# Performance work log

Hardware: AMD Instinct MI355X
Metric: run time of the kernel (lower is better)

## Reference

```python
import jax, jax.numpy as jnp
import numpy as np

N = 10000      # nodes
E = 320000     # edges (avg degree 32)
D_IN = 128
D_H = 256
D_C = 32       # comm_dim
D_OUT = 64


def setup_inputs() -> dict:
    key = jax.random.key(0)
    ks = jax.random.split(key, 14)
    p = lambda k, shape: jax.random.normal(k, shape, jnp.float32) * 0.02
    return {
        "x": jax.random.normal(ks[0], (N, D_IN), jnp.float32),
        "edge_index": jax.random.randint(ks[1], (2, E), 0, N),
        "W_in": p(ks[2], (D_IN, D_H)), "b_in": jnp.zeros((D_H,), jnp.float32),
        "Wq": p(ks[3], (D_H, D_C)),   "bq": jnp.zeros((D_C,), jnp.float32),
        "Wk": p(ks[4], (D_H, D_C)),   "bk": jnp.zeros((D_C,), jnp.float32),
        "Wv": p(ks[5], (D_H, D_H)),   "bv": jnp.zeros((D_H,), jnp.float32),
        "W1": p(ks[6], (2 * D_H, D_H)), "b1": jnp.zeros((D_H,), jnp.float32),
        "W2": p(ks[7], (D_H, D_OUT)),  "b2": jnp.zeros((D_OUT,), jnp.float32),
    }


def reference(x, edge_index, W_in, b_in, Wq, bq, Wk, bk, Wv, bv, W1, b1, W2, b2):
    n = x.shape[0]
    h = x @ W_in + b_in                       # [N, D_H]
    q = h @ Wq + bq                           # [N, D_C]
    k = h @ Wk + bk                           # [N, D_C]
    v = h @ Wv + bv                           # [N, D_H]
    scores = (q @ k.T) / np.sqrt(q.shape[-1]).astype(np.float32)  # [N, N]
    # torch: zeros -> scatter 1 at edges -> masked_fill(==0, -inf);
    # edge positions keep value 1.0 ADDED to scores (faithful quirk).
    mask = jnp.full((n, n), -jnp.inf, jnp.float32)
    mask = mask.at[edge_index[0], edge_index[1]].set(1.0)
    w = jax.nn.softmax(scores + mask, axis=-1)
    w = jnp.nan_to_num(w, nan=0.0)            # rows with no edges -> all zeros
    comm = w @ v                              # [N, D_H]
    combined = jnp.concatenate([h, comm], axis=-1)  # [N, 2*D_H]
    return jax.nn.relu(combined @ W1 + b1) @ W2 + b2  # [N, D_OUT]
```

## Files before the change

### kernel.cpp

```cpp
#include <hip/hip_runtime.h>
#include <stdint.h>
#include <stddef.h>

constexpr int N_NODES = 10000;
constexpr int N_EDGES = 320000;
constexpr int DIM_IN  = 128;
constexpr int DIM_H   = 256;
constexpr int DIM_C   = 32;
constexpr int DIM_OUT = 64;
constexpr int DIM_QKV = DIM_C + DIM_C + DIM_H;
constexpr int DIM_QK  = 2 * DIM_C;
constexpr int DIM_CAT = 2 * DIM_H;
constexpr float SCALE = 0.17677669529663687f;
constexpr int MAXD = 192;
constexpr float VSCALE = 64.0f;
constexpr int PAD2 = 72;
constexpr int HP   = 264;

#if __has_builtin(__builtin_amdgcn_cvt_pk_f32_fp8) && __has_builtin(__builtin_amdgcn_cvt_pk_f32_fp8)
#define V_FP8 1
#else
#define V_FP8 0
#endif

constexpr size_t alignw(size_t w) { return (w + 15) & ~size_t(15); }
constexpr size_t OFF_DEG   = 0;
constexpr size_t OFF_COL   = alignw(OFF_DEG + N_NODES);
constexpr size_t OFF_QK    = alignw(OFF_COL + (size_t)N_NODES * MAXD);
constexpr size_t OFF_VT    = alignw(OFF_QK + (size_t)N_NODES * DIM_QK);
constexpr size_t OFF_CATBF = alignw(OFF_VT + (size_t)N_NODES * DIM_H / 2);
constexpr size_t OFF_WINT  = alignw(OFF_CATBF + (size_t)N_NODES * DIM_CAT / 2);
constexpr size_t OFF_WQKVT = alignw(OFF_WINT + (size_t)DIM_H * DIM_IN / 2);
constexpr size_t OFF_W1T   = alignw(OFF_WQKVT + (size_t)DIM_QKV * DIM_H / 2);
constexpr size_t OFF_W2T   = alignw(OFF_W1T + (size_t)DIM_H * DIM_CAT / 2);

typedef __attribute__((ext_vector_type(8))) short short8;
typedef __attribute__((ext_vector_type(4))) float floatx4;
typedef __attribute__((ext_vector_type(2))) float floatx2;

#define MFMA16 __builtin_amdgcn_mfma_f32_16x16x32_bf16

__device__ inline unsigned short f2bf(float f) {
    uint32_t u = __builtin_bit_cast(uint32_t, f);
    uint32_t r = (u + 0x7fffu + ((u >> 16) & 1u)) >> 16;
    return (unsigned short)r;
}
__device__ inline float bf2f_lo(uint32_t u) { return __builtin_bit_cast(float, u << 16); }
__device__ inline float bf2f_hi(uint32_t u) { return __builtin_bit_cast(float, u & 0xffff0000u); }

__global__ void prep_w(const float* __restrict__ W_in,
                       const float* __restrict__ Wq, const float* __restrict__ Wk,
                       const float* __restrict__ Wv,
                       int* __restrict__ deg,
                       unsigned short* __restrict__ WinT, unsigned short* __restrict__ WqkvT)
{
    const int i0 = blockIdx.x * blockDim.x + threadIdx.x;
    const int stride = gridDim.x * blockDim.x;
    for (int i = i0; i < N_NODES; i += stride) deg[i] = 0;
    for (int idx = i0; idx < DIM_IN * DIM_H; idx += stride) {
        int k = idx >> 8, n = idx & 255;
        WinT[n * DIM_IN + k] = f2bf(W_in[idx]);
    }
    for (int idx = i0; idx < DIM_H * DIM_C; idx += stride) {
        int k = idx >> 5, n = idx & 31;
        WqkvT[n * DIM_H + k] = f2bf(Wq[idx]);
    }
    for (int idx = i0; idx < DIM_H * DIM_C; idx += stride) {
        int k = idx >> 5, n = idx & 31;
        WqkvT[(DIM_C + n) * DIM_H + k] = f2bf(Wk[idx]);
    }
    for (int idx = i0; idx < DIM_H * DIM_H; idx += stride) {
        int k = idx >> 8, n = idx & 255;
        WqkvT[(2 * DIM_C + n) * DIM_H + k] = f2bf(Wv[idx]);
    }
}

__global__ __launch_bounds__(256)
void gemm12(const float* __restrict__ x, const int* __restrict__ ei,
            const unsigned short* __restrict__ WinT, const float* __restrict__ b_in,
            const unsigned short* __restrict__ WqkvT,
            const float* __restrict__ bq, const float* __restrict__ bk,
            const float* __restrict__ bv,
            const float* __restrict__ W1, const float* __restrict__ W2,
            int* __restrict__ deg, int* __restrict__ col,
            unsigned short* __restrict__ cat_bf, float* __restrict__ qk,
            unsigned short* __restrict__ v_tab,
            unsigned short* __restrict__ W1T, unsigned short* __restrict__ W2T)
{
    __shared__ alignas(16) char SMEM[62976];
    short* hS  = (short*)SMEM;
    short* As1 = (short*)(SMEM + 16896);
    short* Bs1 = (short*)(SMEM + 21504);
    short* Bs2 = (short*)(SMEM + 16896);
    const int tid   = threadIdx.x;
    const int bid   = blockIdx.x;
    const int wave  = tid >> 6;
    const int lane  = tid & 63;
    const int quad  = lane >> 4;
    const int col16 = lane & 15;
    const int sr    = tid >> 3;
    const int sc    = (tid & 7) * 8;
    const int row0  = bid * 32;
    const int gr_s  = row0 + sr;

    float4 xa = {}, xb = {};
    if (gr_s < N_NODES) {
        const float4* xp = (const float4*)(x + (size_t)gr_s * DIM_IN + sc);
        xa = xp[0]; xb = xp[1];
    }
    short8 wreg[8];
    #pragma unroll
    for (int p = 0; p < 8; ++p)
        wreg[p] = *(const short8*)(WinT + (size_t)(sr + p * 32) * DIM_IN + sc);

    short8 breg[10];
    floatx4 acc[2][4] = {};
    #pragma unroll
    for (int k0 = 0; k0 < DIM_IN; k0 += 64) {
        {
            uint4 o;
            o.x = (uint32_t)f2bf(xa.x) | ((uint32_t)f2bf(xa.y) << 16);
            o.y = (uint32_t)f2bf(xa.z) | ((uint32_t)f2bf(xa.w) << 16);
            o.z = (uint32_t)f2bf(xb.x) | ((uint32_t)f2bf(xb.y) << 16);
            o.w = (uint32_t)f2bf(xb.z) | ((uint32_t)f2bf(xb.w) << 16);
            *(uint4*)(As1 + sr * PAD2 + sc) = o;
        }
        #pragma unroll
        for (int p = 0; p < 8; ++p)
            *(short8*)(Bs1 + (sr + p * 32) * PAD2 + sc) = wreg[p];
        if (k0 + 64 < DIM_IN) {
            xa = {}; xb = {};
            if (gr_s < N_NODES) {
                const float4* xp = (const float4*)(x + (size_t)gr_s * DIM_IN + (k0 + 64) + sc);
                xa = xp[0]; xb = xp[1];
            }
            #pragma unroll
            for (int p = 0; p < 8; ++p)
                wreg[p] = *(const short8*)(WinT + (size_t)(sr + p * 32) * DIM_IN + (k0 + 64) + sc);
        } else {
            #pragma unroll
            for (int p = 0; p < 10; ++p)
                breg[p] = *(const short8*)(WqkvT + (size_t)(sr + p * 32) * DIM_H + sc);
        }
        __syncthreads();
        short8 af[2][2], bfr[4][2];
        #pragma unroll
        for (int m = 0; m < 2; ++m)
            #pragma unroll
            for (int kh = 0; kh < 2; ++kh)
                af[m][kh] = *(const short8*)(As1 + (m * 16 + col16) * PAD2 + kh * 32 + quad * 8);
        #pragma unroll
        for (int n = 0; n < 4; ++n)
            #pragma unroll
            for (int kh = 0; kh < 2; ++kh)
                bfr[n][kh] = *(const short8*)(Bs1 + (wave * 64 + n * 16 + col16) * PAD2 + kh * 32 + quad * 8);
        #pragma unroll
        for (int m = 0; m < 2; ++m)
            #pragma unroll
            for (int n = 0; n < 4; ++n)
                #pragma unroll
                for (int kh = 0; kh < 2; ++kh)
                    acc[m][n] = MFMA16(af[m][kh], bfr[n][kh], acc[m][n], 0, 0, 0);
        __syncthreads();
    }
    #pragma unroll
    for (int m = 0; m < 2; ++m)
        #pragma unroll
        for (int n = 0; n < 4; ++n) {
            int gc = wave * 64 + n * 16 + col16;
            float bia = b_in[gc];
            #pragma unroll
            for (int r = 0; r < 4; ++r) {
                int lr = m * 16 + quad * 4 + r;
                unsigned short hv = f2bf(acc[m][n][r] + bia);
                hS[lr * HP + gc] = (short)hv;
                if (row0 + lr < N_NODES) cat_bf[(size_t)(row0 + lr) * DIM_CAT + gc] = hv;
            }
        }
    __syncthreads();

    floatx4 acc2[2][5] = {};
    #pragma unroll
    for (int k0 = 0; k0 < DIM_H; k0 += 64) {
        #pragma unroll
        for (int p = 0; p < 10; ++p)
            *(short8*)(Bs2 + (sr + p * 32) * PAD2 + sc) = breg[p];
        if (k0 + 64 < DIM_H) {
            #pragma unroll
            for (int p = 0; p < 10; ++p)
                breg[p] = *(const short8*)(WqkvT + (size_t)(sr + p * 32) * DIM_H + (k0 + 64) + sc);
        }
        __syncthreads();
        short8 af[2][2], bfr[5][2];
        #pragma unroll
        for (int m = 0; m < 2; ++m)
            #pragma unroll
            for (int kh = 0; kh < 2; ++kh)
                af[m][kh] = *(const short8*)(hS + (m * 16 + col16) * HP + k0 + kh * 32 + quad * 8);
        #pragma unroll
        for (int n = 0; n < 5; ++n)
            #pragma unroll
            for (int kh = 0; kh < 2; ++kh)
                bfr[n][kh] = *(const short8*)(Bs2 + (wave * 80 + n * 16 + col16) * PAD2 + kh * 32 + quad * 8);
        #pragma unroll
        for (int m = 0; m < 2; ++m)
            #pragma unroll
            for (int n = 0; n < 5; ++n)
                #pragma unroll
                for (int kh = 0; kh < 2; ++kh)
                    acc2[m][n] = MFMA16(af[m][kh], bfr[n][kh], acc2[m][n], 0, 0, 0);
        __syncthreads();
    }
    #pragma unroll
    for (int m = 0; m < 2; ++m)
        #pragma unroll
        for (int n = 0; n < 5; ++n) {
            int gc = wave * 80 + n * 16 + col16;
            float bia = (gc < DIM_C) ? bq[gc] : (gc < DIM_QK) ? bk[gc - DIM_C] : bv[gc - DIM_QK];
            #pragma unroll
            for (int r = 0; r < 4; ++r) {
                int gr = row0 + m * 16 + quad * 4 + r;
                if (gr >= N_NODES) continue;
                float v = acc2[m][n][r] + bia;
                if (gc < DIM_QK) {
                    qk[(size_t)gr * DIM_QK + gc] = v;
                } else {
#if V_FP8
                    int pk = __builtin_amdgcn_cvt_pk_fp8_f32(v * VSCALE, 0.f, 0, false);
                    ((unsigned char*)v_tab)[(size_t)gr * DIM_H + (gc - DIM_QK)] =
                        (unsigned char)(pk & 0xff);
#else
                    v_tab[(size_t)gr * DIM_H + (gc - DIM_QK)] = f2bf(v);
#endif
                }
            }
        }

    {
        const int stride = gridDim.x * 256;
        const int i0 = bid * 256 + tid;
        int s4[4], d4[4]; bool ok[4];
        #pragma unroll
        for (int t = 0; t < 4; ++t) {
            int e = i0 + t * stride;
            ok[t] = e < N_EDGES;
            s4[t] = ok[t] ? ei[e] : 0;
            d4[t] = ok[t] ? ei[N_EDGES + e] : 0;
        }
        #pragma unroll
        for (int t = 0; t < 4; ++t)
            if (ok[t]) {
                int slot = atomicAdd(&deg[s4[t]], 1);
                if (slot < MAXD) col[s4[t] * MAXD + slot] = d4[t];
            }
        for (int idx = i0; idx < DIM_CAT * DIM_H; idx += stride) {
            int k = idx >> 8, n = idx & 255;
            W1T[n * DIM_CAT + k] = f2bf(W1[idx]);
        }
        for (int idx = i0; idx < DIM_H * DIM_OUT; idx += stride) {
            int k = idx >> 6, n = idx & 63;
            W2T[n * DIM_H + k] = f2bf(W2[idx]);
        }
    }
}

__global__ __launch_bounds__(256)
void attn_row(const float* __restrict__ qk, const unsigned short* __restrict__ v_tab,
              const int* __restrict__ deg, const int* __restrict__ col,
              unsigned short* __restrict__ cat_bf) {
    __shared__ alignas(16) int dstS[4][MAXD];
    __shared__ float wS[4][MAXD];
    __shared__ float qS[4][DIM_C];
    const int wave = threadIdx.x >> 6;
    const int lane = threadIdx.x & 63;
    const int row = blockIdx.x * 4 + wave;
    int d = deg[row];
    if (d > MAXD) d = MAXD;
    const int* crow = col + (size_t)row * MAXD;

    for (int p = lane; p < d; p += 64) dstS[wave][p] = crow[p];
    if (lane < DIM_C) qS[wave][lane] = qk[(size_t)row * DIM_QK + lane];
    __syncthreads();

    float mysum = 0.f;
    if (d <= 64) {
        int mydst = (lane < d) ? dstS[wave][lane] : -1;
        bool dup = false;
        {
            const int4* ds4 = (const int4*)(&dstS[wave][0]);
            const int lim = (lane < d) ? lane : 0;
            for (int j0 = 0; j0 < lim; j0 += 4) {
                int4 v = ds4[j0 >> 2];
                dup = dup || (v.x == mydst)
                   || (j0 + 1 < lim && v.y == mydst)
                   || (j0 + 2 < lim && v.z == mydst)
                   || (j0 + 3 < lim && v.w == mydst);
            }
        }
        float w = 0.f;
        if (lane < d && !dup) {
            const float4* kp = (const float4*)(qk + (size_t)mydst * DIM_QK + DIM_C);
            float s = 0.f;
            #pragma unroll
            for (int i = 0; i < DIM_C / 4; ++i) {
                float4 b = kp[i];
                s += qS[wave][4 * i + 0] * b.x + qS[wave][4 * i + 1] * b.y
                   + qS[wave][4 * i + 2] * b.z + qS[wave][4 * i + 3] * b.w;
            }
            w = expf(s * SCALE);
        }
        wS[wave][lane] = w;
        mysum = w;
    } else {
        for (int p = lane; p < d; p += 64) {
            int mydst = dstS[wave][p];
            bool dup = false;
            for (int j = 0; j < p; ++j) dup = dup || (dstS[wave][j] == mydst);
            float w = 0.f;
            if (!dup) {
                const float4* kp = (const float4*)(qk + (size_t)mydst * DIM_QK + DIM_C);
                float s = 0.f;
                #pragma unroll
                for (int i = 0; i < DIM_C / 4; ++i) {
                    float4 b = kp[i];
                    s += qS[wave][4 * i + 0] * b.x + qS[wave][4 * i + 1] * b.y
                       + qS[wave][4 * i + 2] * b.z + qS[wave][4 * i + 3] * b.w;
                }
                w = expf(s * SCALE);
            }
            wS[wave][p] = w;
            mysum += w;
        }
    }
    #pragma unroll
    for (int off = 32; off; off >>= 1) mysum += __shfl_down(mysum, off, 64);
    float total = __shfl(mysum, 0, 64);
#if V_FP8
    float inv = (d > 0 && total > 0.f) ? 1.0f / (total * VSCALE) : 0.f;
#else
    float inv = (d > 0 && total > 0.f) ? 1.0f / total : 0.f;
#endif
    __syncthreads();

    float4 acc = make_float4(0.f, 0.f, 0.f, 0.f);
#if V_FP8
    const uint32_t* vb = (const uint32_t*)v_tab;
#else
    const uint2* vb = (const uint2*)v_tab;
#endif
    for (int p0 = 0; p0 < d; p0 += 16) {
        int j[16]; float w[16];
        #pragma unroll
        for (int t = 0; t < 16; ++t) {
            int idx = p0 + t;
            bool in = idx < d;
            j[t] = in ? dstS[wave][idx] : 0;
            w[t] = in ? wS[wave][idx] : 0.f;
        }
#if V_FP8
        uint32_t r[16];
        #pragma unroll
        for (int t = 0; t < 16; ++t) r[t] = vb[(size_t)j[t] * 64 + lane];
        #pragma unroll
        for (int t = 0; t < 16; ++t) {
            floatx2 lo = __builtin_amdgcn_cvt_pk_f32_fp8(r[t], false);
            floatx2 hi = __builtin_amdgcn_cvt_pk_f32_fp8(r[t], true);
            acc.x += w[t] * lo.x; acc.y += w[t] * lo.y;
            acc.z += w[t] * hi.x; acc.w += w[t] * hi.y;
        }
#else
        uint2 r[16];
        #pragma unroll
        for (int t = 0; t < 16; ++t) r[t] = vb[(size_t)j[t] * 64 + lane];
        #pragma unroll
        for (int t = 0; t < 16; ++t) {
            acc.x += w[t] * bf2f_lo(r[t].x);
            acc.y += w[t] * bf2f_hi(r[t].x);
            acc.z += w[t] * bf2f_lo(r[t].y);
            acc.w += w[t] * bf2f_hi(r[t].y);
        }
#endif
    }
    acc.x *= inv; acc.y *= inv; acc.z *= inv; acc.w *= inv;
    uint2 o;
    o.x = (uint32_t)f2bf(acc.x) | ((uint32_t)f2bf(acc.y) << 16);
    o.y = (uint32_t)f2bf(acc.z) | ((uint32_t)f2bf(acc.w) << 16);
    *(uint2*)(cat_bf + (size_t)row * DIM_CAT + DIM_H + lane * 4) = o;
}

__global__ __launch_bounds__(256)
void gemm_w1w2(const unsigned short* __restrict__ cat, const unsigned short* __restrict__ W1T,
               const float* __restrict__ b1, const unsigned short* __restrict__ W2T,
               const float* __restrict__ b2, float* __restrict__ out, int M)
{
    constexpr int TP = 260;
    __shared__ short As[32 * PAD2];
    __shared__ short BsTs[256 * PAD2];
    short* Bs = BsTs;
    short* Ts = BsTs;
    const int tid   = threadIdx.x;
    const int wave  = tid >> 6;
    const int lane  = tid & 63;
    const int quad  = lane >> 4;
    const int col16 = lane & 15;
    const int row0  = blockIdx.x * 32;

    const int sr = tid >> 3;
    const int sc = (tid & 7) * 8;
    const int gr_s = row0 + sr;

    short8 areg = {};
    if (gr_s < M) areg = *(const short8*)(cat + (size_t)gr_s * DIM_CAT + sc);
    short8 breg[8];
    #pragma unroll
    for (int p = 0; p < 8; ++p)
        breg[p] = *(const short8*)(W1T + (size_t)(sr + p * 32) * DIM_CAT + sc);

    floatx4 acc[2][4] = {};
    #pragma unroll
    for (int k0 = 0; k0 < DIM_CAT; k0 += 64) {
        *(short8*)(As + sr * PAD2 + sc) = areg;
        #pragma unroll
        for (int p = 0; p < 8; ++p)
            *(short8*)(Bs + (sr + p * 32) * PAD2 + sc) = breg[p];
        if (k0 + 64 < DIM_CAT) {
            areg = short8{};
            if (gr_s < M) areg = *(const short8*)(cat + (size_t)gr_s * DIM_CAT + (k0 + 64) + sc);
            #pragma unroll
            for (int p = 0; p < 8; ++p)
                breg[p] = *(const short8*)(W1T + (size_t)(sr + p * 32) * DIM_CAT + (k0 + 64) + sc);
        }
        __syncthreads();
        short8 af[2][2], bfr[4][2];
        #pragma unroll
        for (int m = 0; m < 2; ++m)
            #pragma unroll
            for (int kh = 0; kh < 2; ++kh)
                af[m][kh] = *(const short8*)(As + (m * 16 + col16) * PAD2 + kh * 32 + quad * 8);
        #pragma unroll
        for (int n = 0; n < 4; ++n)
            #pragma unroll
            for (int kh = 0; kh < 2; ++kh)
                bfr[n][kh] = *(const short8*)(Bs + (wave * 64 + n * 16 + col16) * PAD2 + kh * 32 + quad * 8);
        #pragma unroll
        for (int m = 0; m < 2; ++m)
            #pragma unroll
            for (int n = 0; n < 4; ++n)
                #pragma unroll
                for (int kh = 0; kh < 2; ++kh)
                    acc[m][n] = MFMA16(af[m][kh], bfr[n][kh], acc[m][n], 0, 0, 0);
        __syncthreads();
    }

    #pragma unroll
    for (int m = 0; m < 2; ++m)
        #pragma unroll
        for (int n = 0; n < 4; ++n) {
            int gc = wave * 64 + n * 16 + col16;
            float bia = b1[gc];
            #pragma unroll
            for (int r = 0; r < 4; ++r) {
                int lr = m * 16 + quad * 4 + r;
                Ts[lr * TP + gc] = (short)f2bf(fmaxf(acc[m][n][r] + bia, 0.f));
            }
        }
    __syncthreads();

    floatx4 acc2[2] = {};
    #pragma unroll
    for (int k0 = 0; k0 < DIM_H; k0 += 32) {
        short8 b = *(const short8*)(W2T + (size_t)(wave * 16 + col16) * DIM_H + k0 + quad * 8);
        #pragma unroll
        for (int m = 0; m < 2; ++m) {
            short8 a = *(const short8*)(Ts + (m * 16 + col16) * TP + k0 + quad * 8);
            acc2[m] = MFMA16(a, b, acc2[m], 0, 0, 0);
        }
    }
    #pragma unroll
    for (int m = 0; m < 2; ++m) {
        int gc = wave * 16 + col16;
        float bia = b2[gc];
        #pragma unroll
        for (int r = 0; r < 4; ++r) {
            int gr = row0 + m * 16 + quad * 4 + r;
            if (gr < M) out[(size_t)gr * DIM_OUT + gc] = acc2[m][r] + bia;
        }
    }
}

extern "C" void kernel_launch(void* const* d_in, const int* in_sizes, int n_in,
                              void* d_out, int out_size, void* d_ws, size_t ws_size,
                              hipStream_t stream) {
    (void)in_sizes; (void)n_in; (void)out_size; (void)ws_size;
    const float* x    = (const float*)d_in[0];
    const int*   ei   = (const int*)d_in[1];
    const float* W_in = (const float*)d_in[2];
    const float* b_in = (const float*)d_in[3];
    const float* Wq   = (const float*)d_in[4];
    const float* bq   = (const float*)d_in[5];
    const float* Wk   = (const float*)d_in[6];
    const float* bk   = (const float*)d_in[7];
    const float* Wv   = (const float*)d_in[8];
    const float* bv   = (const float*)d_in[9];
    const float* W1   = (const float*)d_in[10];
    const float* b1   = (const float*)d_in[11];
    const float* W2   = (const float*)d_in[12];
    const float* b2   = (const float*)d_in[13];
    float* out = (float*)d_out;

    uint32_t* ws      = (uint32_t*)d_ws;
    int*      deg     = (int*)(ws + OFF_DEG);
    int*      col     = (int*)(ws + OFF_COL);
    float*    qk      = (float*)(ws + OFF_QK);
    unsigned short* v_tab  = (unsigned short*)(ws + OFF_VT);
    unsigned short* cat_bf = (unsigned short*)(ws + OFF_CATBF);
    unsigned short* WinT   = (unsigned short*)(ws + OFF_WINT);
    unsigned short* WqkvT  = (unsigned short*)(ws + OFF_WQKVT);
    unsigned short* W1T    = (unsigned short*)(ws + OFF_W1T);
    unsigned short* W2T    = (unsigned short*)(ws + OFF_W2T);

    prep_w<<<256, 256, 0, stream>>>(W_in, Wq, Wk, Wv, deg, WinT, WqkvT);
    gemm12<<<(N_NODES + 31) / 32, 256, 0, stream>>>(
        x, ei, WinT, b_in, WqkvT, bq, bk, bv, W1, W2,
        deg, col, cat_bf, qk, v_tab, W1T, W2T);
    attn_row<<<N_NODES / 4, 256, 0, stream>>>(qk, v_tab, deg, col, cat_bf);
    gemm_w1w2<<<(N_NODES + 31) / 32, 256, 0, stream>>>(
        cat_bf, W1T, b1, W2T, b2, out, N_NODES);
}
```

Measured before the change: 162.1 us.

## Fold W_in into QKV and W1 weights to skip materializing h

Exploits linearity: h = x·W_in + b_in is never formed. A prep kernel precomputes W_in·[Wq|Wk|Wv] and W_in·W1[:256], plus the matching effective biases. The QKV GEMM then runs with K=128 directly on x, and the W1 GEMM uses K=384 over x and comm. This removes the h GEMM and the cat buffer writes, but adds a small fp32 weight-product prep and changes bf16 rounding, since the product is rounded once instead of h being rounded.

New measurement: 165.6 us. 1.02x slower.

```diff
diff --git a/kernel.cpp b/kernel.cpp
--- a/kernel.cpp
+++ b/kernel.cpp
@@ -10,14 +10,13 @@
 constexpr int DIM_OUT = 64;
 constexpr int DIM_QKV = DIM_C + DIM_C + DIM_H;
 constexpr int DIM_QK  = 2 * DIM_C;
-constexpr int DIM_CAT = 2 * DIM_H;
+constexpr int K_W1    = DIM_IN + DIM_H;
 constexpr float SCALE = 0.17677669529663687f;
 constexpr int MAXD = 192;
 constexpr float VSCALE = 64.0f;
 constexpr int PAD2 = 72;
-constexpr int HP   = 264;
-
-#if __has_builtin(__builtin_amdgcn_cvt_pk_f32_fp8) && __has_builtin(__builtin_amdgcn_cvt_pk_f32_fp8)
+
+#if __has_builtin(__builtin_amdgcn_cvt_pk_f32_fp8) && __has_builtin(__builtin_amdgcn_cvt_pk_fp8_f32)
 #define V_FP8 1
 #else
 #define V_FP8 0
@@ -28,11 +27,12 @@
 constexpr size_t OFF_COL   = alignw(OFF_DEG + N_NODES);
 constexpr size_t OFF_QK    = alignw(OFF_COL + (size_t)N_NODES * MAXD);
 constexpr size_t OFF_VT    = alignw(OFF_QK + (size_t)N_NODES * DIM_QK);
-constexpr size_t OFF_CATBF = alignw(OFF_VT + (size_t)N_NODES * DIM_H / 2);
-constexpr size_t OFF_WINT  = alignw(OFF_CATBF + (size_t)N_NODES * DIM_CAT / 2);
-constexpr size_t OFF_WQKVT = alignw(OFF_WINT + (size_t)DIM_H * DIM_IN / 2);
-constexpr size_t OFF_W1T   = alignw(OFF_WQKVT + (size_t)DIM_QKV * DIM_H / 2);
-constexpr size_t OFF_W2T   = alignw(OFF_W1T + (size_t)DIM_H * DIM_CAT / 2);
+constexpr size_t OFF_CMB   = alignw(OFF_VT + (size_t)N_NODES * DIM_H / 2);
+constexpr size_t OFF_WEFF  = alignw(OFF_CMB + (size_t)N_NODES * DIM_H / 2);
+constexpr size_t OFF_W1BIG = alignw(OFF_WEFF + (size_t)DIM_QKV * DIM_IN / 2);
+constexpr size_t OFF_W2T   = alignw(OFF_W1BIG + (size_t)DIM_H * K_W1 / 2);
+constexpr size_t OFF_BEFF  = alignw(OFF_W2T + (size_t)DIM_OUT * DIM_H / 2);
+constexpr size_t OFF_B1EFF = alignw(OFF_BEFF + DIM_QKV);
 
 typedef __attribute__((ext_vector_type(8))) short short8;
 typedef __attribute__((ext_vector_type(4))) float floatx4;
@@ -48,50 +48,87 @@
 __device__ inline float bf2f_lo(uint32_t u) { return __builtin_bit_cast(float, u << 16); }
 __device__ inline float bf2f_hi(uint32_t u) { return __builtin_bit_cast(float, u & 0xffff0000u); }
 
-__global__ void prep_w(const float* __restrict__ W_in,
-                       const float* __restrict__ Wq, const float* __restrict__ Wk,
-                       const float* __restrict__ Wv,
-                       int* __restrict__ deg,
-                       unsigned short* __restrict__ WinT, unsigned short* __restrict__ WqkvT)
+__global__ __launch_bounds__(320)
+void prep(const float* __restrict__ W_in,
+          const float* __restrict__ Wq, const float* __restrict__ Wk,
+          const float* __restrict__ Wv,
+          const float* __restrict__ bq, const float* __restrict__ bk,
+          const float* __restrict__ bv, const float* __restrict__ b_in,
+          const float* __restrict__ W1, const float* __restrict__ b1,
+          const float* __restrict__ W2,
+          int* __restrict__ deg,
+          unsigned short* __restrict__ WeffT, unsigned short* __restrict__ W1big,
+          unsigned short* __restrict__ W2T,
+          float* __restrict__ b_eff, float* __restrict__ b1_eff)
 {
-    const int i0 = blockIdx.x * blockDim.x + threadIdx.x;
-    const int stride = gridDim.x * blockDim.x;
-    for (int i = i0; i < N_NODES; i += stride) deg[i] = 0;
-    for (int idx = i0; idx < DIM_IN * DIM_H; idx += stride) {
-        int k = idx >> 8, n = idx & 255;
-        WinT[n * DIM_IN + k] = f2bf(W_in[idx]);
-    }
-    for (int idx = i0; idx < DIM_H * DIM_C; idx += stride) {
-        int k = idx >> 5, n = idx & 31;
-        WqkvT[n * DIM_H + k] = f2bf(Wq[idx]);
-    }
-    for (int idx = i0; idx < DIM_H * DIM_C; idx += stride) {
-        int k = idx >> 5, n = idx & 31;
-        WqkvT[(DIM_C + n) * DIM_H + k] = f2bf(Wk[idx]);
-    }
-    for (int idx = i0; idx < DIM_H * DIM_H; idx += stride) {
-        int k = idx >> 8, n = idx & 255;
-        WqkvT[(2 * DIM_C + n) * DIM_H + k] = f2bf(Wv[idx]);
+    const int bid = blockIdx.x;
+    const int tid = threadIdx.x;
+    if (bid < 128) {
+        const int k = bid, n = tid;
+        float acc = 0.f;
+        const float* wrow = W_in + (size_t)k * DIM_H;
+        if (n < DIM_C) {
+            for (int j = 0; j < DIM_H; ++j) acc += wrow[j] * Wq[j * DIM_C + n];
+        } else if (n < DIM_QK) {
+            for (int j = 0; j < DIM_H; ++j) acc += wrow[j] * Wk[j * DIM_C + (n - DIM_C)];
+        } else {
+            for (int j = 0; j < DIM_H; ++j) acc += wrow[j] * Wv[j * DIM_H + (n - DIM_QK)];
+        }
+        WeffT[n * DIM_IN + k] = f2bf(acc);
+    } else if (bid < 256) {
+        const int k = bid - 128, n = tid;
+        if (n < DIM_H) {
+            float acc = 0.f;
+            const float* wrow = W_in + (size_t)k * DIM_H;
+            for (int j = 0; j < DIM_H; ++j) acc += wrow[j] * W1[(size_t)j * DIM_H + n];
+            W1big[n * K_W1 + k] = f2bf(acc);
+        }
+    } else if (bid < 288) {
+        for (int idx = (bid - 256) * 320 + tid; idx < DIM_H * DIM_H; idx += 32 * 320) {
+            int jj = idx >> 8, n = idx & 255;
+            W1big[n * K_W1 + DIM_IN + jj] = f2bf(W1[(size_t)(DIM_H + jj) * DIM_H + n]);
+        }
+    } else if (bid < 296) {
+        for (int idx = (bid - 288) * 320 + tid; idx < DIM_H * DIM_OUT; idx += 8 * 320) {
+            int k = idx >> 6, n = idx & 63;
+            W2T[n * DIM_H + k] = f2bf(W2[(size_t)k * DIM_OUT + n]);
+        }
+    } else if (bid == 296) {
+        const int n = tid;
+        float acc;
+        if (n < DIM_C) {
+            acc = bq[n];
+            for (int j = 0; j < DIM_H; ++j) acc += b_in[j] * Wq[j * DIM_C + n];
+        } else if (n < DIM_QK) {
+            acc = bk[n - DIM_C];
+            for (int j = 0; j < DIM_H; ++j) acc += b_in[j] * Wk[j * DIM_C + (n - DIM_C)];
+        } else {
+            acc = bv[n - DIM_QK];
+            for (int j = 0; j < DIM_H; ++j) acc += b_in[j] * Wv[j * DIM_H + (n - DIM_QK)];
+        }
+        b_eff[n] = acc;
+    } else if (bid == 297) {
+        const int n = tid;
+        if (n < DIM_H) {
+            float acc = b1[n];
+            for (int j = 0; j < DIM_H; ++j) acc += b_in[j] * W1[(size_t)j * DIM_H + n];
+            b1_eff[n] = acc;
+        }
+    } else {
+        int i = (bid - 298) * 320 + tid;
+        if (i < N_NODES) deg[i] = 0;
     }
 }
 
 __global__ __launch_bounds__(256)
-void gemm12(const float* __restrict__ x, const int* __restrict__ ei,
-            const unsigned short* __restrict__ WinT, const float* __restrict__ b_in,
-            const unsigned short* __restrict__ WqkvT,
-            const float* __restrict__ bq, const float* __restrict__ bk,
-            const float* __restrict__ bv,
-            const float* __restrict__ W1, const float* __restrict__ W2,
-            int* __restrict__ deg, int* __restrict__ col,
-            unsigned short* __restrict__ cat_bf, float* __restrict__ qk,
-            unsigned short* __restrict__ v_tab,
-            unsigned short* __restrict__ W1T, unsigned short* __restrict__ W2T)
+void gemm_qkv(const float* __restrict__ x, const int* __restrict__ ei,
+              const unsigned short* __restrict__ WeffT, const float* __restrict__ b_eff,
+              int* __restrict__ deg, int* __restrict__ col,
+              float* __restrict__ qk, unsigned short* __restrict__ v_tab)
 {
-    __shared__ alignas(16) char SMEM[62976];
-    short* hS  = (short*)SMEM;
-    short* As1 = (short*)(SMEM + 16896);
-    short* Bs1 = (short*)(SMEM + 21504);
-    short* Bs2 = (short*)(SMEM + 16896);
+    __shared__ alignas(16) char SMEM[50688];
+    short* As = (short*)SMEM;
+    short* Bs = (short*)(SMEM + 4608);
     const int tid   = threadIdx.x;
     const int bid   = blockIdx.x;
     const int wave  = tid >> 6;
@@ -108,13 +145,12 @@
         const float4* xp = (const float4*)(x + (size_t)gr_s * DIM_IN + sc);
         xa = xp[0]; xb = xp[1];
     }
-    short8 wreg[8];
-    #pragma unroll
-    for (int p = 0; p < 8; ++p)
-        wreg[p] = *(const short8*)(WinT + (size_t)(sr + p * 32) * DIM_IN + sc);
-
-    short8 breg[10];
-    floatx4 acc[2][4] = {};
+    short8 wreg[10];
+    #pragma unroll
+    for (int p = 0; p < 10; ++p)
+        wreg[p] = *(const short8*)(WeffT + (size_t)(sr + p * 32) * DIM_IN + sc);
+
+    floatx4 acc[2][5] = {};
     #pragma unroll
     for (int k0 = 0; k0 < DIM_IN; k0 += 64) {
         {
@@ -123,11 +159,11 @@
             o.y = (uint32_t)f2bf(xa.z) | ((uint32_t)f2bf(xa.w) << 16);
             o.z = (uint32_t)f2bf(xb.x) | ((uint32_t)f2bf(xb.y) << 16);
             o.w = (uint32_t)f2bf(xb.z) | ((uint32_t)f2bf(xb.w) << 16);
-            *(uint4*)(As1 + sr * PAD2 + sc) = o;
-        }
-        #pragma unroll
-        for (int p = 0; p < 8; ++p)
-            *(short8*)(Bs1 + (sr + p * 32) * PAD2 + sc) = wreg[p];
+            *(uint4*)(As + sr * PAD2 + sc) = o;
+        }
+        #pragma unroll
+        for (int p = 0; p < 10; ++p)
+            *(short8*)(Bs + (sr + p * 32) * PAD2 + sc) = wreg[p];
         if (k0 + 64 < DIM_IN) {
             xa = {}; xb = {};
             if (gr_s < N_NODES) {
@@ -135,29 +171,25 @@
                 xa = xp[0]; xb = xp[1];
             }
             #pragma unroll
-            for (int p = 0; p < 8; ++p)
-                wreg[p] = *(const short8*)(WinT + (size_t)(sr + p * 32) * DIM_IN + (k0 + 64) + sc);
-        } else {
-            #pragma unroll
             for (int p = 0; p < 10; ++p)
-                breg[p] = *(const short8*)(WqkvT + (size_t)(sr + p * 32) * DIM_H + sc);
+                wreg[p] = *(const short8*)(WeffT + (size_t)(sr + p * 32) * DIM_IN + (k0 + 64) + sc);
         }
         __syncthreads();
-        short8 af[2][2], bfr[4][2];
+        short8 af[2][2], bfr[5][2];
         #pragma unroll
         for (int m = 0; m < 2; ++m)
             #pragma unroll
             for (int kh = 0; kh < 2; ++kh)
-                af[m][kh] = *(const short8*)(As1 + (m * 16 + col16) * PAD2 + kh * 32 + quad * 8);
-        #pragma unroll
-        for (int n = 0; n < 4; ++n)
+                af[m][kh] = *(const short8*)(As + (m * 16 + col16) * PAD2 + kh * 32 + quad * 8);
+        #pragma unroll
+        for (int n = 0; n < 5; ++n)
             #pragma unroll
             for (int kh = 0; kh < 2; ++kh)
-                bfr[n][kh] = *(const short8*)(Bs1 + (wave * 64 + n * 16 + col16) * PAD2 + kh * 32 + quad * 8);
+                bfr[n][kh] = *(const short8*)(Bs + (wave * 80 + n * 16 + col16) * PAD2 + kh * 32 + quad * 8);
         #pragma unroll
         for (int m = 0; m < 2; ++m)
             #pragma unroll
-            for (int n = 0; n < 4; ++n)
+            for (int n = 0; n < 5; ++n)
                 #pragma unroll
                 for (int kh = 0; kh < 2; ++kh)
                     acc[m][n] = MFMA16(af[m][kh], bfr[n][kh], acc[m][n], 0, 0, 0);
@@ -166,62 +198,14 @@
     #pragma unroll
     for (int m = 0; m < 2; ++m)
         #pragma unroll
-        for (int n = 0; n < 4; ++n) {
-            int gc = wave * 64 + n * 16 + col16;
-            float bia = b_in[gc];
-            #pragma unroll
-            for (int r = 0; r < 4; ++r) {
-                int lr = m * 16 + quad * 4 + r;
-                unsigned short hv = f2bf(acc[m][n][r] + bia);
-                hS[lr * HP + gc] = (short)hv;
-                if (row0 + lr < N_NODES) cat_bf[(size_t)(row0 + lr) * DIM_CAT + gc] = hv;
-            }
-        }
-    __syncthreads();
-
-    floatx4 acc2[2][5] = {};
-    #pragma unroll
-    for (int k0 = 0; k0 < DIM_H; k0 += 64) {
-        #pragma unroll
-        for (int p = 0; p < 10; ++p)
-            *(short8*)(Bs2 + (sr + p * 32) * PAD2 + sc) = breg[p];
-        if (k0 + 64 < DIM_H) {
-            #pragma unroll
-            for (int p = 0; p < 10; ++p)
-                breg[p] = *(const short8*)(WqkvT + (size_t)(sr + p * 32) * DIM_H + (k0 + 64) + sc);
-        }
-        __syncthreads();
-        short8 af[2][2], bfr[5][2];
-        #pragma unroll
-        for (int m = 0; m < 2; ++m)
-            #pragma unroll
-            for (int kh = 0; kh < 2; ++kh)
-                af[m][kh] = *(const short8*)(hS + (m * 16 + col16) * HP + k0 + kh * 32 + quad * 8);
-        #pragma unroll
-        for (int n = 0; n < 5; ++n)
-            #pragma unroll
-            for (int kh = 0; kh < 2; ++kh)
-                bfr[n][kh] = *(const short8*)(Bs2 + (wave * 80 + n * 16 + col16) * PAD2 + kh * 32 + quad * 8);
-        #pragma unroll
-        for (int m = 0; m < 2; ++m)
-            #pragma unroll
-            for (int n = 0; n < 5; ++n)
-                #pragma unroll
-                for (int kh = 0; kh < 2; ++kh)
-                    acc2[m][n] = MFMA16(af[m][kh], bfr[n][kh], acc2[m][n], 0, 0, 0);
-        __syncthreads();
-    }
-    #pragma unroll
-    for (int m = 0; m < 2; ++m)
-        #pragma unroll
         for (int n = 0; n < 5; ++n) {
             int gc = wave * 80 + n * 16 + col16;
-            float bia = (gc < DIM_C) ? bq[gc] : (gc < DIM_QK) ? bk[gc - DIM_C] : bv[gc - DIM_QK];
+            float bia = b_eff[gc];
             #pragma unroll
             for (int r = 0; r < 4; ++r) {
                 int gr = row0 + m * 16 + quad * 4 + r;
                 if (gr >= N_NODES) continue;
-                float v = acc2[m][n][r] + bia;
+                float v = acc[m][n][r] + bia;
                 if (gc < DIM_QK) {
                     qk[(size_t)gr * DIM_QK + gc] = v;
                 } else {
@@ -253,21 +237,13 @@
                 int slot = atomicAdd(&deg[s4[t]], 1);
                 if (slot < MAXD) col[s4[t] * MAXD + slot] = d4[t];
             }
-        for (int idx = i0; idx < DIM_CAT * DIM_H; idx += stride) {
-            int k = idx >> 8, n = idx & 255;
-            W1T[n * DIM_CAT + k] = f2bf(W1[idx]);
-        }
-        for (int idx = i0; idx < DIM_H * DIM_OUT; idx += stride) {
-            int k = idx >> 6, n = idx & 63;
-            W2T[n * DIM_H + k] = f2bf(W2[idx]);
-        }
     }
 }
 
 __global__ __launch_bounds__(256)
 void attn_row(const float* __restrict__ qk, const unsigned short* __restrict__ v_tab,
               const int* __restrict__ deg, const int* __restrict__ col,
-              unsigned short* __restrict__ cat_bf) {
+              unsigned short* __restrict__ comm_bf) {
     __shared__ alignas(16) int dstS[4][MAXD];
     __shared__ float wS[4][MAXD];
     __shared__ float qS[4][DIM_C];
@@ -385,13 +361,14 @@
     uint2 o;
     o.x = (uint32_t)f2bf(acc.x) | ((uint32_t)f2bf(acc.y) << 16);
     o.y = (uint32_t)f2bf(acc.z) | ((uint32_t)f2bf(acc.w) << 16);
-    *(uint2*)(cat_bf + (size_t)row * DIM_CAT + DIM_H + lane * 4) = o;
+    *(uint2*)(comm_bf + (size_t)row * DIM_H + lane * 4) = o;
 }
 
 __global__ __launch_bounds__(256)
-void gemm_w1w2(const unsigned short* __restrict__ cat, const unsigned short* __restrict__ W1T,
-               const float* __restrict__ b1, const unsigned short* __restrict__ W2T,
-               const float* __restrict__ b2, float* __restrict__ out, int M)
+void gemm_w1w2(const float* __restrict__ x, const unsigned short* __restrict__ comm_bf,
+               const unsigned short* __restrict__ W1big, const float* __restrict__ b1_eff,
+               const unsigned short* __restrict__ W2T, const float* __restrict__ b2,
+               float* __restrict__ out, int M)
 {
     constexpr int TP = 260;
     __shared__ short As[32 * PAD2];
@@ -409,26 +386,49 @@
     const int sc = (tid & 7) * 8;
     const int gr_s = row0 + sr;
 
-    short8 areg = {};
-    if (gr_s < M) areg = *(const short8*)(cat + (size_t)gr_s * DIM_CAT + sc);
+    float4 xa = {}, xb = {};
+    if (gr_s < M) {
+        const float4* xp = (const float4*)(x + (size_t)gr_s * DIM_IN + sc);
+        xa = xp[0]; xb = xp[1];
+    }
+    short8 acm = {};
     short8 breg[8];
     #pragma unroll
     for (int p = 0; p < 8; ++p)
-        breg[p] = *(const short8*)(W1T + (size_t)(sr + p * 32) * DIM_CAT + sc);
+        breg[p] = *(const short8*)(W1big + (size_t)(sr + p * 32) * K_W1 + sc);
 
     floatx4 acc[2][4] = {};
     #pragma unroll
-    for (int k0 = 0; k0 < DIM_CAT; k0 += 64) {
-        *(short8*)(As + sr * PAD2 + sc) = areg;
+    for (int ks = 0; ks < 6; ++ks) {
+        const int k0 = ks * 64;
+        if (ks < 2) {
+            uint4 o;
+            o.x = (uint32_t)f2bf(xa.x) | ((uint32_t)f2bf(xa.y) << 16);
+            o.y = (uint32_t)f2bf(xa.z) | ((uint32_t)f2bf(xa.w) << 16);
+            o.z = (uint32_t)f2bf(xb.x) | ((uint32_t)f2bf(xb.y) << 16);
+            o.w = (uint32_t)f2bf(xb.z) | ((uint32_t)f2bf(xb.w) << 16);
+            *(uint4*)(As + sr * PAD2 + sc) = o;
+        } else {
+            *(short8*)(As + sr * PAD2 + sc) = acm;
+        }
         #pragma unroll
         for (int p = 0; p < 8; ++p)
             *(short8*)(Bs + (sr + p * 32) * PAD2 + sc) = breg[p];
-        if (k0 + 64 < DIM_CAT) {
-            areg = short8{};
-            if (gr_s < M) areg = *(const short8*)(cat + (size_t)gr_s * DIM_CAT + (k0 + 64) + sc);
+        if (ks == 0) {
+            xa = {}; xb = {};
+            if (gr_s < M) {
+                const float4* xp = (const float4*)(x + (size_t)gr_s * DIM_IN + 64 + sc);
+                xa = xp[0]; xb = xp[1];
+            }
+        } else if (ks < 5) {
+            acm = short8{};
+            if (gr_s < M)
+                acm = *(const short8*)(comm_bf + (size_t)gr_s * DIM_H + (k0 + 64 - DIM_IN) + sc);
+        }
+        if (ks < 5) {
             #pragma unroll
             for (int p = 0; p < 8; ++p)
-                breg[p] = *(const short8*)(W1T + (size_t)(sr + p * 32) * DIM_CAT + (k0 + 64) + sc);
+                breg[p] = *(const short8*)(W1big + (size_t)(sr + p * 32) * K_W1 + (k0 + 64) + sc);
         }
         __syncthreads();
         short8 af[2][2], bfr[4][2];
@@ -457,7 +457,7 @@
         #pragma unroll
         for (int n = 0; n < 4; ++n) {
             int gc = wave * 64 + n * 16 + col16;
-            float bia = b1[gc];
+            float bia = b1_eff[gc];
             #pragma unroll
             for (int r = 0; r < 4; ++r) {
                 int lr = m * 16 + quad * 4 + r;
@@ -513,17 +513,18 @@
     int*      col     = (int*)(ws + OFF_COL);
     float*    qk      = (float*)(ws + OFF_QK);
     unsigned short* v_tab  = (unsigned short*)(ws + OFF_VT);
-    unsigned short* cat_bf = (unsigned short*)(ws + OFF_CATBF);
-    unsigned short* WinT   = (unsigned short*)(ws + OFF_WINT);
-    unsigned short* WqkvT  = (unsigned short*)(ws + OFF_WQKVT);
-    unsigned short* W1T    = (unsigned short*)(ws + OFF_W1T);
+    unsigned short* comm_bf= (unsigned short*)(ws + OFF_CMB);
+    unsigned short* WeffT  = (unsigned short*)(ws + OFF_WEFF);
+    unsigned short* W1big  = (unsigned short*)(ws + OFF_W1BIG);
     unsigned short* W2T    = (unsigned short*)(ws + OFF_W2T);
-
-    prep_w<<<256, 256, 0, stream>>>(W_in, Wq, Wk, Wv, deg, WinT, WqkvT);
-    gemm12<<<(N_NODES + 31) / 32, 256, 0, stream>>>(
-        x, ei, WinT, b_in, WqkvT, bq, bk, bv, W1, W2,
-        deg, col, cat_bf, qk, v_tab, W1T, W2T);
-    attn_row<<<N_NODES / 4, 256, 0, stream>>>(qk, v_tab, deg, col, cat_bf);
+    float*    b_eff   = (float*)(ws + OFF_BEFF);
+    float*    b1_eff  = (float*)(ws + OFF_B1EFF);
+
+    prep<<<330, 320, 0, stream>>>(W_in, Wq, Wk, Wv, bq, bk, bv, b_in, W1, b1, W2,
+                                  deg, WeffT, W1big, W2T, b_eff, b1_eff);
+    gemm_qkv<<<(N_NODES + 31) / 32, 256, 0, stream>>>(
+        x, ei, WeffT, b_eff, deg, col, qk, v_tab);
+    attn_row<<<N_NODES / 4, 256, 0, stream>>>(qk, v_tab, deg, col, comm_bf);
     gemm_w1w2<<<(N_NODES + 31) / 32, 256, 0, stream>>>(
-        cat_bf, W1T, b1, W2T, b2, out, N_NODES);
+        x, comm_bf, W1big, b1_eff, W2T, b2, out, N_NODES);
 }
```
